# Performance work log

Hardware: AMD Instinct MI355X
Metric: run time of the kernel (lower is better)

The kernel has to match this reference:

```python
import jax, jax.numpy as jnp
import numpy as np

N = 10000       # nodes
E = 160000      # edges (avg degree 16)
IN_C = 16       # node in_channels
IN_E = 8        # edge in_edge_channels
DIMS = [32, 16, 16, 16]   # hidden_dims
ENN_H = 128     # edge_nn_hidden
EMLP_H = 16     # edge_mlp_hidden


def setup_inputs() -> dict:
    key = jax.random.key(0)
    ks = iter(jax.random.split(key, 80))
    def rn(shape, s=0.1):
        return jax.random.normal(next(ks), shape, dtype=jnp.float32) * s
    inp = {}
    inp['x'] = jax.random.normal(next(ks), (N, IN_C), dtype=jnp.float32)
    inp['edge_attr'] = jax.random.normal(next(ks), (E, IN_E), dtype=jnp.float32)
    inp['edge_index'] = jax.random.randint(next(ks), (2, E), 0, N, dtype=jnp.int32)
    in_dims = [IN_C] + DIMS[:-1]
    for i, (di, do) in enumerate(zip(in_dims, DIMS)):
        inp[f'p_w{i}'] = rn((do, di));            inp[f'p_b{i}'] = rn((do,))
        inp[f'e1_w{i}'] = rn((ENN_H, IN_E));      inp[f'e1_b{i}'] = rn((ENN_H,))
        inp[f'e2_w{i}'] = rn((do * do, ENN_H), 0.02); inp[f'e2_b{i}'] = rn((do * do,), 0.02)
        inp[f'r_w{i}'] = rn((do, do));            inp[f'c_b{i}'] = rn((do,))
    inp['m_w0'] = rn((EMLP_H, DIMS[-1])); inp['m_b0'] = rn((EMLP_H,))
    inp['m_w1'] = rn((1, EMLP_H));        inp['m_b1'] = rn((1,))
    return inp


def _forward(x, edge_attr, edge_index, params, m_w0, m_b0, m_w1, m_b1):
    row, col = edge_index[0], edge_index[1]
    n = x.shape[0]
    # in-degree for scatter-mean (clamped to 1, as PyG scatter mean)
    deg = jnp.clip(jax.ops.segment_sum(jnp.ones(row.shape[0], jnp.float32), col, num_segments=n), 1.0)
    for (pw, pb, ew1, eb1, ew2, eb2, rw, cb) in params:
        d = pw.shape[0]
        x_proj = x @ pw.T + pb                                    # [N, d]
        # edge-conditioned weight matrices: [E, d, d]
        W = (jax.nn.relu(edge_attr @ ew1.T + eb1) @ ew2.T + eb2).reshape(-1, d, d)
        msg = jnp.einsum('ei,eio->eo', x_proj[row], W)            # [E, d]
        agg = jax.ops.segment_sum(msg, col, num_segments=n) / deg[:, None]
        conv = agg + x_proj @ rw.T + cb                           # NNConv: aggr + root + bias
        x = jax.nn.relu(conv) + x_proj                            # relu + skip
    edge_repr = x[row] + x[col]                                   # [E, d_last]
    out = jax.nn.relu(edge_repr @ m_w0.T + m_b0) @ m_w1.T + m_b1  # [E, 1]
    return out[:, 0]


def reference(x, edge_attr, edge_index,
              p_w0, p_b0, e1_w0, e1_b0, e2_w0, e2_b0, r_w0, c_b0,
              p_w1, p_b1, e1_w1, e1_b1, e2_w1, e2_b1, r_w1, c_b1,
              p_w2, p_b2, e1_w2, e1_b2, e2_w2, e2_b2, r_w2, c_b2,
              p_w3, p_b3, e1_w3, e1_b3, e2_w3, e2_b3, r_w3, c_b3,
              m_w0, m_b0, m_w1, m_b1):
    params = [
        (p_w0, p_b0, e1_w0, e1_b0, e2_w0, e2_b0, r_w0, c_b0),
        (p_w1, p_b1, e1_w1, e1_b1, e2_w1, e2_b1, r_w1, c_b1),
        (p_w2, p_b2, e1_w2, e1_b2, e2_w2, e2_b2, r_w2, c_b2),
        (p_w3, p_b3, e1_w3, e1_b3, e2_w3, e2_b3, r_w3, c_b3),
    ]
    return _forward(x, edge_attr, edge_index, params, m_w0, m_b0, m_w1, m_b1)
```

## Files before the change

### kernel.cpp

```cpp
#include <hip/hip_runtime.h>

#define NN 10000
#define NE 160000
static constexpr int TPB = 256;
static constexpr int SCAN_T = 1024;

typedef unsigned int uint32;

static __device__ __forceinline__ ushort f2bf(float f) {
  uint32 u = __float_as_uint(f);
  u += 0x7fff + ((u >> 16) & 1);
  return (ushort)(u >> 16);
}
static __device__ __forceinline__ uint32 pk2bf(float a, float b) {
  return (uint32)f2bf(a) | ((uint32)f2bf(b) << 16);
}
static __device__ __forceinline__ void dot2bf(float& acc, uint32 a, uint32 b) {
  asm("v_dot2_f32_bf16 %0, %1, %2, %0" : "+v"(acc) : "v"(a), "v"(b));
}


__global__ void k_count(const int* __restrict__ ei, int* __restrict__ cnt) {
  int e = blockIdx.x * TPB + threadIdx.x;
  if (e >= NE) return;
  atomicAdd(&cnt[ei[e]], 1);
  atomicAdd(&cnt[NN + ei[NE + e]], 1);
}

__global__ void __launch_bounds__(SCAN_T)
k_scan2(const int* __restrict__ cnt_all, int* __restrict__ off_r, int* __restrict__ cur_r,
        int* __restrict__ off_c, int* __restrict__ cur_c) {
  const int* cnt = (blockIdx.x == 0) ? cnt_all : cnt_all + NN;
  int* off = (blockIdx.x == 0) ? off_r : off_c;
  int* cur = (blockIdx.x == 0) ? cur_r : cur_c;
  __shared__ int s_wave[16];
  __shared__ int s_carry;
  int tid = threadIdx.x;
  int lane = tid & 63, wid = tid >> 6;
  if (tid == 0) s_carry = 0;
  __syncthreads();
  for (int base = 0; base < NN; base += SCAN_T) {
    int i = base + tid;
    int v = (i < NN) ? cnt[i] : 0;
    int s = v;
    #pragma unroll
    for (int d = 1; d < 64; d <<= 1) {
      int t = __shfl_up(s, d, 64);
      if (lane >= d) s += t;
    }
    if (lane == 63) s_wave[wid] = s;
    __syncthreads();
    if (wid == 0 && lane < 16) {
      int ws = s_wave[lane];
      #pragma unroll
      for (int d = 1; d < 16; d <<= 1) {
        int t = __shfl_up(ws, d, 64);
        if (lane >= d) ws += t;
      }
      s_wave[lane] = ws;
    }
    __syncthreads();
    int waveoff = (wid > 0) ? s_wave[wid - 1] : 0;
    int excl = s_carry + waveoff + s - v;
    if (i < NN) { off[i] = excl; cur[i] = excl; }
    __syncthreads();
    if (tid == 0) s_carry += s_wave[15];
    __syncthreads();
  }
  if (tid == 0) off[NN] = s_carry;
}

__global__ void k_fill_row(const int* __restrict__ ei, int* __restrict__ cur_row,
                           int* __restrict__ eid_row) {
  int e = blockIdx.x * TPB + threadIdx.x;
  if (e >= NE) return;
  int r = ei[e];
  int p = atomicAdd(&cur_row[r], 1);
  eid_row[p] = e;
}

__global__ void k_fill_colpos(const int* __restrict__ ei, const int* __restrict__ eid_row,
                              int* __restrict__ cur_col, int* __restrict__ colpos) {
  int s = blockIdx.x * TPB + threadIdx.x;
  if (s >= NE) return;
  int e = eid_row[s];
  int c = ei[NE + e];
  int p = atomicAdd(&cur_col[c], 1);
  colpos[s] = p;
}


template<int DIN, int D>
__global__ void __launch_bounds__(TPB)
k_nodeprep(const float* __restrict__ x, const float* __restrict__ pw, const float* __restrict__ pb,
           const float* __restrict__ rw, const float* __restrict__ cb, const float* __restrict__ eb2,
           float* __restrict__ xp, float* __restrict__ root, float* __restrict__ Bb) {
  __shared__ float s_pw[D * DIN], s_rw[D * D], s_eb2[D * D], s_pb[D], s_cb[D];
  for (int t = threadIdx.x; t < D * DIN; t += TPB) s_pw[t] = pw[t];
  for (int t = threadIdx.x; t < D * D; t += TPB) { s_rw[t] = rw[t]; s_eb2[t] = eb2[t]; }
  for (int t = threadIdx.x; t < D; t += TPB) { s_pb[t] = pb[t]; s_cb[t] = cb[t]; }
  __syncthreads();
  int n = blockIdx.x * TPB + threadIdx.x;
  if (n >= NN) return;
  float xv[DIN];
  const float4* x4 = (const float4*)(x + (size_t)n * DIN);
  #pragma unroll
  for (int i = 0; i < DIN / 4; i++) {
    float4 v = x4[i];
    xv[4*i+0] = v.x; xv[4*i+1] = v.y; xv[4*i+2] = v.z; xv[4*i+3] = v.w;
  }
  float xpv[D];
  #pragma unroll
  for (int o = 0; o < D; o++) {
    float a = s_pb[o];
    #pragma unroll
    for (int i = 0; i < DIN; i++) a = fmaf(s_pw[o*DIN + i], xv[i], a);
    xpv[o] = a;
    xp[(size_t)n*D + o] = a;
  }
  #pragma unroll
  for (int o = 0; o < D; o++) {
    float a = s_cb[o];
    #pragma unroll
    for (int i = 0; i < D; i++) a = fmaf(s_rw[o*D + i], xpv[i], a);
    root[(size_t)n*D + o] = a;
  }
  #pragma unroll
  for (int o = 0; o < D; o++) {
    float a = 0.f;
    #pragma unroll
    for (int i = 0; i < D; i++) a = fmaf(xpv[i], s_eb2[i*D + o], a);
    Bb[(size_t)n*D + o] = a;
  }
}

template<int DP, int D>
__global__ void __launch_bounds__(TPB)
k_aggprep(const int* __restrict__ col_off,
          const float* __restrict__ msg0, const float* __restrict__ msg1,
          const float* __restrict__ root_prev, const float* __restrict__ xp_prev,
          const float* __restrict__ pw, const float* __restrict__ pb,
          const float* __restrict__ rw, const float* __restrict__ cb,
          const float* __restrict__ eb2,
          float* __restrict__ xp, float* __restrict__ root, float* __restrict__ Bb) {
  constexpr int NB = TPB / DP;
  __shared__ float s_x[NB][DP];
  __shared__ float s_xpv[NB][D];
  __shared__ float s_pw[D * DP], s_rw[D * D], s_eb2[D * D], s_pb[D], s_cb[D];
  int tid = threadIdx.x;
  for (int t = tid; t < D * DP; t += TPB) s_pw[t] = pw[t];
  for (int t = tid; t < D * D; t += TPB) { s_rw[t] = rw[t]; s_eb2[t] = eb2[t]; }
  for (int t = tid; t < D; t += TPB) { s_pb[t] = pb[t]; s_cb[t] = cb[t]; }
  int g = tid / DP, o = tid % DP;
  int n = blockIdx.x * NB + g;
  if (n < NN) {
    int p0 = col_off[n], p1 = col_off[n + 1];
    float acc = 0.f;
    for (int p = p0; p < p1; p++)
      acc += msg0[(size_t)p * DP + o] + msg1[(size_t)p * DP + o];
    float deg = (p1 > p0) ? (float)(p1 - p0) : 1.f;
    float conv = acc / deg + root_prev[(size_t)n * DP + o];
    s_x[g][o] = (conv > 0.f ? conv : 0.f) + xp_prev[(size_t)n * DP + o];
  }
  __syncthreads();
  int g2 = tid / D, o2 = tid % D;
  int n2 = blockIdx.x * NB + g2;
  if (g2 < NB && n2 < NN) {
    float a = s_pb[o2];
    #pragma unroll
    for (int i = 0; i < DP; i++) a = fmaf(s_pw[o2 * DP + i], s_x[g2][i], a);
    s_xpv[g2][o2] = a;
    xp[(size_t)n2 * D + o2] = a;
  }
  __syncthreads();
  if (g2 < NB && n2 < NN) {
    float r2 = s_cb[o2], b2 = 0.f;
    #pragma unroll
    for (int i = 0; i < D; i++) {
      r2 = fmaf(s_rw[o2 * D + i], s_xpv[g2][i], r2);
      b2 = fmaf(s_xpv[g2][i], s_eb2[i * D + o2], b2);
    }
    root[(size_t)n2 * D + o2] = r2;
    Bb[(size_t)n2 * D + o2] = b2;
  }
}

__global__ void k_trans_all(const float* __restrict__ e0, const float* __restrict__ e1,
                            const float* __restrict__ e2, const float* __restrict__ e3,
                            uint32* __restrict__ Vp) {
  int t = blockIdx.x * TPB + threadIdx.x;
  const float* ew2; uint32* dst; int D, loc;
  if (t < 65536)       { ew2 = e0; dst = Vp;         D = 32; loc = t; }
  else if (t < 81920)  { ew2 = e1; dst = Vp + 65536; D = 16; loc = t - 65536; }
  else if (t < 98304)  { ew2 = e2; dst = Vp + 81920; D = 16; loc = t - 81920; }
  else if (t < 114688) { ew2 = e3; dst = Vp + 98304; D = 16; loc = t - 98304; }
  else return;
  int COLS = D * 128;
  int i2 = loc / COLS;
  int r = loc - i2 * COLS;
  int w = r >> 1, p = r & 1;
  int k2 = w / D, o = w - k2 * D;
  int k = 2 * k2 + p;
  float lo = ew2[((size_t)((2 * i2) * D + o)) * 128 + k];
  float hi = ew2[((size_t)((2 * i2 + 1) * D + o)) * 128 + k];
  dst[loc] = pk2bf(lo, hi);
}

template<int D, int G>
__global__ void __launch_bounds__(TPB)
k_fused(const int* __restrict__ eid_row, const int* __restrict__ row_off,
        const int* __restrict__ colpos,
        const float* __restrict__ ea, const float* __restrict__ ew1,
        const float* __restrict__ eb1, const uint32* __restrict__ Vp,
        const float* __restrict__ xp, const float* __restrict__ Bb,
        float* __restrict__ msg0, float* __restrict__ msg1) {
  constexpr int OQ = D / 4;
  constexpr int EB = TPB / OQ;
  constexpr int COLS = D * 128;
  constexpr int UW = COLS / 2;
  constexpr int UH = UW / 2;
  constexpr int UP = UH + 4;
  constexpr int CT = UH / TPB;

  __shared__ __align__(16) uint32 s_w1tp[4 * 64];
  __shared__ float  s_b1[64];
  __shared__ __align__(16) uint32 s_U[G * UP];
  __shared__ __align__(16) uint32 s_hp[EB * 34];
  __shared__ __align__(16) uint32 s_eap[EB * 4];
  __shared__ int    s_cp[EB];
  __shared__ uint32 s_xp2[G][D / 2];
  __shared__ float  s_B[G * D];
  __shared__ int    s_off[G + 1];

  int tid = threadIdx.x;
  int half = blockIdx.y;
  int n0 = blockIdx.x * G;
  int GA = NN - n0; if (GA > G) GA = G;
  float* msgH = half ? msg1 : msg0;

  for (int t = tid; t < 4 * 64; t += TPB) {
    int i2 = t >> 6, kloc = t & 63;
    int k = half * 64 + kloc;
    s_w1tp[t] = pk2bf(ew1[k * 8 + 2 * i2], ew1[k * 8 + 2 * i2 + 1]);
  }
  for (int t = tid; t < 64; t += TPB) s_b1[t] = eb1[half * 64 + t];
  for (int t = tid; t < G * (D / 2); t += TPB) {
    int g = t / (D / 2), i2 = t % (D / 2);
    if (g < GA) {
      float2 v = *(const float2*)(xp + (size_t)(n0 + g) * D + 2 * i2);
      s_xp2[g][i2] = pk2bf(v.x, v.y);
    } else {
      s_xp2[g][i2] = 0;
    }
  }
  for (int t = tid; t < G * D; t += TPB) {
    int g = t / D, i = t % D;
    s_B[t] = (g < GA && half == 0) ? Bb[(size_t)(n0 + g) * D + i] : 0.f;
  }
  if (tid <= GA) s_off[tid] = row_off[n0 + tid];
  __syncthreads();

  {
    const uint2* Vp2 = (const uint2*)Vp;
    float accLo[G][CT], accHi[G][CT];
    #pragma unroll
    for (int g = 0; g < G; g++)
      #pragma unroll
      for (int j = 0; j < CT; j++) { accLo[g][j] = 0.f; accHi[g][j] = 0.f; }
    #pragma unroll 2
    for (int i2 = 0; i2 < D / 2; i2++) {
      uint2 vv[CT];
      #pragma unroll
      for (int j = 0; j < CT; j++)
        vv[j] = Vp2[(size_t)i2 * UW + half * UH + j * TPB + tid];
      #pragma unroll
      for (int g = 0; g < G; g++) {
        uint32 xg = s_xp2[g][i2];
        #pragma unroll
        for (int j = 0; j < CT; j++) {
          dot2bf(accLo[g][j], xg, vv[j].x);
          dot2bf(accHi[g][j], xg, vv[j].y);
        }
      }
    }
    #pragma unroll
    for (int g = 0; g < G; g++)
      #pragma unroll
      for (int j = 0; j < CT; j++)
        s_U[g * UP + j * TPB + tid] = pk2bf(accLo[g][j], accHi[g][j]);
  }

  int p0 = row_off[n0], p1 = row_off[n0 + GA];
  int el = tid / OQ, oq = tid % OQ;
  for (int pc = p0; pc < p1; pc += EB) {
    int cnt = p1 - pc; if (cnt > EB) cnt = EB;
    __syncthreads();
    for (int t = tid; t < cnt * 4; t += TPB) {
      int e2 = t >> 2, i2 = t & 3;
      float2 v = *(const float2*)(ea + (size_t)eid_row[pc + e2] * 8 + 2 * i2);
      s_eap[t] = pk2bf(v.x, v.y);
    }
    for (int t = tid; t < cnt; t += TPB) s_cp[t] = colpos[pc + t];
    __syncthreads();
    for (int t = tid; t < cnt * 32; t += TPB) {
      int e2 = t >> 5, k2 = t & 31;
      float a0 = s_b1[2 * k2], a1 = s_b1[2 * k2 + 1];
      #pragma unroll
      for (int i2 = 0; i2 < 4; i2++) {
        uint32 ep = s_eap[e2 * 4 + i2];
        uint2 ww = *(const uint2*)(s_w1tp + i2 * 64 + 2 * k2);
        dot2bf(a0, ep, ww.x);
        dot2bf(a1, ep, ww.y);
      }
      s_hp[e2 * 34 + k2] = pk2bf(fmaxf(a0, 0.f), fmaxf(a1, 0.f));
    }
    __syncthreads();
    if (el < cnt) {
      int s = pc + el;
      int g = 0;
      #pragma unroll
      for (int q = 1; q < G; q++) g += (q < GA && s >= s_off[q]) ? 1 : 0;
      const uint32* up = s_U + g * UP + oq * 4;
      const uint32* hp = s_hp + el * 34;
      float a0 = 0.f, a1 = 0.f, a2 = 0.f, a3 = 0.f;
      #pragma unroll 4
      for (int k4 = 0; k4 < 16; k4++) {
        uint2 hw = *(const uint2*)(hp + 2 * k4);
        uint4 u0 = *(const uint4*)(up + (2 * k4) * D);
        uint4 u1 = *(const uint4*)(up + (2 * k4 + 1) * D);
        dot2bf(a0, hw.x, u0.x); dot2bf(a1, hw.x, u0.y);
        dot2bf(a2, hw.x, u0.z); dot2bf(a3, hw.x, u0.w);
        dot2bf(a0, hw.y, u1.x); dot2bf(a1, hw.y, u1.y);
        dot2bf(a2, hw.y, u1.z); dot2bf(a3, hw.y, u1.w);
      }
      float4 b = ((const float4*)(s_B + g * D))[oq];
      float4 o4 = {a0 + b.x, a1 + b.y, a2 + b.z, a3 + b.w};
      ((float4*)(msgH + (size_t)s_cp[el] * D))[oq] = o4;
    }
  }
}

template<int D>
__global__ void __launch_bounds__(TPB)
k_agg(const int* __restrict__ col_off,
      const float* __restrict__ msg0, const float* __restrict__ msg1,
      const float* __restrict__ root, const float* __restrict__ xp,
      float* __restrict__ xout) {
  constexpr int GP = TPB / D;
  int g = threadIdx.x / D, o = threadIdx.x % D;
  int n = blockIdx.x * GP + g;
  if (n >= NN) return;
  int p0 = col_off[n], p1 = col_off[n + 1];
  float acc = 0.f;
  for (int p = p0; p < p1; p++) {
    acc += msg0[(size_t)p * D + o] + msg1[(size_t)p * D + o];
  }
  float deg = (p1 > p0) ? (float)(p1 - p0) : 1.f;
  float conv = acc / deg + root[(size_t)n * D + o];
  float rl = conv > 0.f ? conv : 0.f;
  xout[(size_t)n * D + o] = rl + xp[(size_t)n * D + o];
}

__global__ void __launch_bounds__(TPB)
k_final(const int* __restrict__ ei, const float* __restrict__ x,
        const float* __restrict__ mw0, const float* __restrict__ mb0,
        const float* __restrict__ mw1, const float* __restrict__ mb1,
        float* __restrict__ out) {
  __shared__ float s_w0[256], s_b0[16], s_w1[16], s_b1;
  for (int t = threadIdx.x; t < 256; t += TPB) s_w0[t] = mw0[t];
  if (threadIdx.x < 16) { s_b0[threadIdx.x] = mb0[threadIdx.x]; s_w1[threadIdx.x] = mw1[threadIdx.x]; }
  if (threadIdx.x == 0) s_b1 = mb1[0];
  __syncthreads();
  int e = blockIdx.x * TPB + threadIdx.x;
  if (e >= NE) return;
  int r = ei[e], c = ei[NE + e];
  const float4* xr4 = (const float4*)(x + (size_t)r * 16);
  const float4* xc4 = (const float4*)(x + (size_t)c * 16);
  float er[16];
  #pragma unroll
  for (int q = 0; q < 4; q++) {
    float4 vr = xr4[q], vc = xc4[q];
    er[4*q+0] = vr.x + vc.x; er[4*q+1] = vr.y + vc.y;
    er[4*q+2] = vr.z + vc.z; er[4*q+3] = vr.w + vc.w;
  }
  float o = s_b1;
  #pragma unroll
  for (int j = 0; j < 16; j++) {
    float t = s_b0[j];
    #pragma unroll
    for (int k = 0; k < 16; k++) t = fmaf(er[k], s_w0[j * 16 + k], t);
    t = fmaxf(t, 0.f);
    o = fmaf(t, s_w1[j], o);
  }
  out[e] = o;
}


struct LayerPtrs {
  const float *pw, *pb, *ew1, *eb1, *ew2, *eb2, *rw, *cb;
};

extern "C" void kernel_launch(void* const* d_in, const int* in_sizes, int n_in,
                              void* d_out, int out_size, void* d_ws, size_t ws_size,
                              hipStream_t stream) {
  (void)in_sizes; (void)n_in; (void)out_size; (void)ws_size;
  const float* x0 = (const float*)d_in[0];
  const float* ea = (const float*)d_in[1];
  const int* ei = (const int*)d_in[2];
  LayerPtrs L[4];
  for (int l = 0; l < 4; l++) {
    L[l].pw  = (const float*)d_in[3 + 8 * l];
    L[l].pb  = (const float*)d_in[4 + 8 * l];
    L[l].ew1 = (const float*)d_in[5 + 8 * l];
    L[l].eb1 = (const float*)d_in[6 + 8 * l];
    L[l].ew2 = (const float*)d_in[7 + 8 * l];
    L[l].eb2 = (const float*)d_in[8 + 8 * l];
    L[l].rw  = (const float*)d_in[9 + 8 * l];
    L[l].cb  = (const float*)d_in[10 + 8 * l];
  }
  const float* mw0 = (const float*)d_in[35];
  const float* mb0 = (const float*)d_in[36];
  const float* mw1 = (const float*)d_in[37];
  const float* mb1 = (const float*)d_in[38];
  float* out = (float*)d_out;

  char* w = (char*)d_ws;
  size_t off = 0;
  auto alloc = [&](size_t b) -> void* {
    void* p = w + off;
    off = (off + b + 255) & ~(size_t)255;
    return p;
  };
  int* cnt      = (int*)alloc(sizeof(int) * 2 * NN);
  int* row_off  = (int*)alloc(sizeof(int) * (NN + 1));
  int* col_off  = (int*)alloc(sizeof(int) * (NN + 1));
  int* cur_row  = (int*)alloc(sizeof(int) * NN);
  int* cur_col  = (int*)alloc(sizeof(int) * NN);
  int* eid_row  = (int*)alloc(sizeof(int) * NE);
  int* colpos   = (int*)alloc(sizeof(int) * NE);
  float* xpA   = (float*)alloc(sizeof(float) * NN * 32);
  float* xpB   = (float*)alloc(sizeof(float) * NN * 32);
  float* rootA = (float*)alloc(sizeof(float) * NN * 32);
  float* rootB = (float*)alloc(sizeof(float) * NN * 32);
  float* Bb    = (float*)alloc(sizeof(float) * NN * 32);
  float* msg0  = (float*)alloc(sizeof(float) * NE * 32);
  float* msg1  = (float*)alloc(sizeof(float) * NE * 32);
  float* xfin  = (float*)alloc(sizeof(float) * NN * 16);
  uint32* Vp   = (uint32*)alloc(sizeof(uint32) * 114688);

  hipMemsetAsync(cnt, 0, sizeof(int) * 2 * NN, stream);
  k_count<<<(NE + TPB - 1) / TPB, TPB, 0, stream>>>(ei, cnt);
  k_scan2<<<2, SCAN_T, 0, stream>>>(cnt, row_off, cur_row, col_off, cur_col);
  k_fill_row<<<(NE + TPB - 1) / TPB, TPB, 0, stream>>>(ei, cur_row, eid_row);
  k_fill_colpos<<<(NE + TPB - 1) / TPB, TPB, 0, stream>>>(ei, eid_row, cur_col, colpos);
  k_trans_all<<<(114688 + TPB - 1) / TPB, TPB, 0, stream>>>(
      L[0].ew2, L[1].ew2, L[2].ew2, L[3].ew2, Vp);

  k_nodeprep<16, 32><<<(NN + TPB - 1) / TPB, TPB, 0, stream>>>(
      x0, L[0].pw, L[0].pb, L[0].rw, L[0].cb, L[0].eb2, xpA, rootA, Bb);
  {
    dim3 gf((NN + 3) / 4, 2);
    k_fused<32, 4><<<gf, TPB, 0, stream>>>(
        eid_row, row_off, colpos, ea, L[0].ew1, L[0].eb1, Vp, xpA, Bb, msg0, msg1);
  }
  k_aggprep<32, 16><<<NN / 8, TPB, 0, stream>>>(
      col_off, msg0, msg1, rootA, xpA,
      L[1].pw, L[1].pb, L[1].rw, L[1].cb, L[1].eb2, xpB, rootB, Bb);
  {
    dim3 gf((NN + 5) / 6, 2);
    k_fused<16, 6><<<gf, TPB, 0, stream>>>(
        eid_row, row_off, colpos, ea, L[1].ew1, L[1].eb1, Vp + 65536, xpB, Bb, msg0, msg1);
  }
  k_aggprep<16, 16><<<NN / 16, TPB, 0, stream>>>(
      col_off, msg0, msg1, rootB, xpB,
      L[2].pw, L[2].pb, L[2].rw, L[2].cb, L[2].eb2, xpA, rootA, Bb);
  {
    dim3 gf((NN + 5) / 6, 2);
    k_fused<16, 6><<<gf, TPB, 0, stream>>>(
        eid_row, row_off, colpos, ea, L[2].ew1, L[2].eb1, Vp + 81920, xpA, Bb, msg0, msg1);
  }
  k_aggprep<16, 16><<<NN / 16, TPB, 0, stream>>>(
      col_off, msg0, msg1, rootA, xpA,
      L[3].pw, L[3].pb, L[3].rw, L[3].cb, L[3].eb2, xpB, rootB, Bb);
  {
    dim3 gf((NN + 5) / 6, 2);
    k_fused<16, 6><<<gf, TPB, 0, stream>>>(
        eid_row, row_off, colpos, ea, L[3].ew1, L[3].eb1, Vp + 98304, xpB, Bb, msg0, msg1);
  }
  k_agg<16><<<(NN * 16 + TPB - 1) / TPB, TPB, 0, stream>>>(
      col_off, msg0, msg1, rootB, xpB, xfin);
  k_final<<<(NE + TPB - 1) / TPB, TPB, 0, stream>>>(ei, xfin, mw0, mb0, mw1, mb1, out);
}
```

Baseline: 302.6 us.

## Store edge messages as packed bf16 and widen fused inner-loop loads

Edge messages written by the fused edge kernel are now packed as bf16 pairs instead of fp32, halving the message buffers. The aggregation kernels read and unpack them with two lanes per thread, and their launch grids are resized to match. The fused kernel's inner loop now uses 128-bit hidden-vector loads with a padded row stride, and layer 0 uses a larger node group. This cuts memory traffic on the message write/read round trip, at the cost of bf16 rounding error in the messages before they are summed.

```diff
diff --git a/kernel.cpp b/kernel.cpp
--- a/kernel.cpp
+++ b/kernel.cpp
@@ -14,6 +14,12 @@
 }
 static __device__ __forceinline__ uint32 pk2bf(float a, float b) {
   return (uint32)f2bf(a) | ((uint32)f2bf(b) << 16);
+}
+static __device__ __forceinline__ float bflo(uint32 u) {
+  return __uint_as_float(u << 16);
+}
+static __device__ __forceinline__ float bfhi(uint32 u) {
+  return __uint_as_float(u & 0xffff0000u);
 }
 static __device__ __forceinline__ void dot2bf(float& acc, uint32 a, uint32 b) {
   asm("v_dot2_f32_bf16 %0, %1, %2, %0" : "+v"(acc) : "v"(a), "v"(b));
@@ -137,13 +143,14 @@
 template<int DP, int D>
 __global__ void __launch_bounds__(TPB)
 k_aggprep(const int* __restrict__ col_off,
-          const float* __restrict__ msg0, const float* __restrict__ msg1,
+          const uint32* __restrict__ msg0p, const uint32* __restrict__ msg1p,
           const float* __restrict__ root_prev, const float* __restrict__ xp_prev,
           const float* __restrict__ pw, const float* __restrict__ pb,
           const float* __restrict__ rw, const float* __restrict__ cb,
           const float* __restrict__ eb2,
           float* __restrict__ xp, float* __restrict__ root, float* __restrict__ Bb) {
-  constexpr int NB = TPB / DP;
+  constexpr int W = DP / 2;
+  constexpr int NB = TPB / W;
   __shared__ float s_x[NB][DP];
   __shared__ float s_xpv[NB][D];
   __shared__ float s_pw[D * DP], s_rw[D * D], s_eb2[D * D], s_pb[D], s_cb[D];
@@ -151,37 +158,50 @@
   for (int t = tid; t < D * DP; t += TPB) s_pw[t] = pw[t];
   for (int t = tid; t < D * D; t += TPB) { s_rw[t] = rw[t]; s_eb2[t] = eb2[t]; }
   for (int t = tid; t < D; t += TPB) { s_pb[t] = pb[t]; s_cb[t] = cb[t]; }
-  int g = tid / DP, o = tid % DP;
+  int g = tid / W, o2 = tid % W;
   int n = blockIdx.x * NB + g;
   if (n < NN) {
     int p0 = col_off[n], p1 = col_off[n + 1];
-    float acc = 0.f;
-    for (int p = p0; p < p1; p++)
-      acc += msg0[(size_t)p * DP + o] + msg1[(size_t)p * DP + o];
+    float ax = 0.f, ay = 0.f;
+    for (int p = p0; p < p1; p++) {
+      uint32 w0 = msg0p[(size_t)p * W + o2];
+      uint32 w1 = msg1p[(size_t)p * W + o2];
+      ax += bflo(w0) + bflo(w1);
+      ay += bfhi(w0) + bfhi(w1);
+    }
     float deg = (p1 > p0) ? (float)(p1 - p0) : 1.f;
-    float conv = acc / deg + root_prev[(size_t)n * DP + o];
-    s_x[g][o] = (conv > 0.f ? conv : 0.f) + xp_prev[(size_t)n * DP + o];
+    float2 rp = *(const float2*)(root_prev + (size_t)n * DP + 2 * o2);
+    float2 xq = *(const float2*)(xp_prev + (size_t)n * DP + 2 * o2);
+    float c0 = ax / deg + rp.x, c1 = ay / deg + rp.y;
+    s_x[g][2 * o2]     = (c0 > 0.f ? c0 : 0.f) + xq.x;
+    s_x[g][2 * o2 + 1] = (c1 > 0.f ? c1 : 0.f) + xq.y;
   }
   __syncthreads();
-  int g2 = tid / D, o2 = tid % D;
-  int n2 = blockIdx.x * NB + g2;
-  if (g2 < NB && n2 < NN) {
-    float a = s_pb[o2];
-    #pragma unroll
-    for (int i = 0; i < DP; i++) a = fmaf(s_pw[o2 * DP + i], s_x[g2][i], a);
-    s_xpv[g2][o2] = a;
-    xp[(size_t)n2 * D + o2] = a;
+  for (int t = tid; t < NB * D; t += TPB) {
+    int g2 = t / D, o = t % D;
+    int n2 = blockIdx.x * NB + g2;
+    if (n2 < NN) {
+      float a = s_pb[o];
+      #pragma unroll
+      for (int i = 0; i < DP; i++) a = fmaf(s_pw[o * DP + i], s_x[g2][i], a);
+      s_xpv[g2][o] = a;
+      xp[(size_t)n2 * D + o] = a;
+    }
   }
   __syncthreads();
-  if (g2 < NB && n2 < NN) {
-    float r2 = s_cb[o2], b2 = 0.f;
-    #pragma unroll
-    for (int i = 0; i < D; i++) {
-      r2 = fmaf(s_rw[o2 * D + i], s_xpv[g2][i], r2);
-      b2 = fmaf(s_xpv[g2][i], s_eb2[i * D + o2], b2);
-    }
-    root[(size_t)n2 * D + o2] = r2;
-    Bb[(size_t)n2 * D + o2] = b2;
+  for (int t = tid; t < NB * D; t += TPB) {
+    int g2 = t / D, o = t % D;
+    int n2 = blockIdx.x * NB + g2;
+    if (n2 < NN) {
+      float r2 = s_cb[o], b2 = 0.f;
+      #pragma unroll
+      for (int i = 0; i < D; i++) {
+        r2 = fmaf(s_rw[o * D + i], s_xpv[g2][i], r2);
+        b2 = fmaf(s_xpv[g2][i], s_eb2[i * D + o], b2);
+      }
+      root[(size_t)n2 * D + o] = r2;
+      Bb[(size_t)n2 * D + o] = b2;
+    }
   }
 }
 
@@ -213,7 +233,7 @@
         const float* __restrict__ ea, const float* __restrict__ ew1,
         const float* __restrict__ eb1, const uint32* __restrict__ Vp,
         const float* __restrict__ xp, const float* __restrict__ Bb,
-        float* __restrict__ msg0, float* __restrict__ msg1) {
+        uint32* __restrict__ msg0p, uint32* __restrict__ msg1p) {
   constexpr int OQ = D / 4;
   constexpr int EB = TPB / OQ;
   constexpr int COLS = D * 128;
@@ -225,7 +245,7 @@
   __shared__ __align__(16) uint32 s_w1tp[4 * 64];
   __shared__ float  s_b1[64];
   __shared__ __align__(16) uint32 s_U[G * UP];
-  __shared__ __align__(16) uint32 s_hp[EB * 34];
+  __shared__ __align__(16) uint32 s_hp[EB * 36];
   __shared__ __align__(16) uint32 s_eap[EB * 4];
   __shared__ int    s_cp[EB];
   __shared__ uint32 s_xp2[G][D / 2];
@@ -236,7 +256,7 @@
   int half = blockIdx.y;
   int n0 = blockIdx.x * G;
   int GA = NN - n0; if (GA > G) GA = G;
-  float* msgH = half ? msg1 : msg0;
+  uint32* msgHp = half ? msg1p : msg0p;
 
   for (int t = tid; t < 4 * 64; t += TPB) {
     int i2 = t >> 6, kloc = t & 63;
@@ -312,30 +332,36 @@
         dot2bf(a0, ep, ww.x);
         dot2bf(a1, ep, ww.y);
       }
-      s_hp[e2 * 34 + k2] = pk2bf(fmaxf(a0, 0.f), fmaxf(a1, 0.f));
+      s_hp[e2 * 36 + k2] = pk2bf(fmaxf(a0, 0.f), fmaxf(a1, 0.f));
     }
     __syncthreads();
     if (el < cnt) {
-      int s = pc + el;
       int g = 0;
-      #pragma unroll
-      for (int q = 1; q < G; q++) g += (q < GA && s >= s_off[q]) ? 1 : 0;
+      {
+        int s = pc + el;
+        #pragma unroll
+        for (int q = 1; q < G; q++) g += (q < GA && s >= s_off[q]) ? 1 : 0;
+      }
       const uint32* up = s_U + g * UP + oq * 4;
-      const uint32* hp = s_hp + el * 34;
+      const uint32* hp = s_hp + el * 36;
       float a0 = 0.f, a1 = 0.f, a2 = 0.f, a3 = 0.f;
-      #pragma unroll 4
-      for (int k4 = 0; k4 < 16; k4++) {
-        uint2 hw = *(const uint2*)(hp + 2 * k4);
-        uint4 u0 = *(const uint4*)(up + (2 * k4) * D);
-        uint4 u1 = *(const uint4*)(up + (2 * k4 + 1) * D);
-        dot2bf(a0, hw.x, u0.x); dot2bf(a1, hw.x, u0.y);
-        dot2bf(a2, hw.x, u0.z); dot2bf(a3, hw.x, u0.w);
-        dot2bf(a0, hw.y, u1.x); dot2bf(a1, hw.y, u1.y);
-        dot2bf(a2, hw.y, u1.z); dot2bf(a3, hw.y, u1.w);
+      #pragma unroll
+      for (int k8 = 0; k8 < 8; k8++) {
+        uint4 hw = *(const uint4*)(hp + 4 * k8);
+        uint4 u0 = *(const uint4*)(up + (4 * k8 + 0) * D);
+        uint4 u1 = *(const uint4*)(up + (4 * k8 + 1) * D);
+        uint4 u2 = *(const uint4*)(up + (4 * k8 + 2) * D);
+        uint4 u3 = *(const uint4*)(up + (4 * k8 + 3) * D);
+        dot2bf(a0, hw.x, u0.x); dot2bf(a1, hw.x, u0.y); dot2bf(a2, hw.x, u0.z); dot2bf(a3, hw.x, u0.w);
+        dot2bf(a0, hw.y, u1.x); dot2bf(a1, hw.y, u1.y); dot2bf(a2, hw.y, u1.z); dot2bf(a3, hw.y, u1.w);
+        dot2bf(a0, hw.z, u2.x); dot2bf(a1, hw.z, u2.y); dot2bf(a2, hw.z, u2.z); dot2bf(a3, hw.z, u2.w);
+        dot2bf(a0, hw.w, u3.x); dot2bf(a1, hw.w, u3.y); dot2bf(a2, hw.w, u3.z); dot2bf(a3, hw.w, u3.w);
       }
       float4 b = ((const float4*)(s_B + g * D))[oq];
-      float4 o4 = {a0 + b.x, a1 + b.y, a2 + b.z, a3 + b.w};
-      ((float4*)(msgH + (size_t)s_cp[el] * D))[oq] = o4;
+      uint2 om;
+      om.x = pk2bf(a0 + b.x, a1 + b.y);
+      om.y = pk2bf(a2 + b.z, a3 + b.w);
+      ((uint2*)(msgHp + (size_t)s_cp[el] * (D / 2)))[oq] = om;
     }
   }
 }
@@ -343,22 +369,28 @@
 template<int D>
 __global__ void __launch_bounds__(TPB)
 k_agg(const int* __restrict__ col_off,
-      const float* __restrict__ msg0, const float* __restrict__ msg1,
+      const uint32* __restrict__ msg0p, const uint32* __restrict__ msg1p,
       const float* __restrict__ root, const float* __restrict__ xp,
       float* __restrict__ xout) {
-  constexpr int GP = TPB / D;
-  int g = threadIdx.x / D, o = threadIdx.x % D;
+  constexpr int W = D / 2;
+  constexpr int GP = TPB / W;
+  int g = threadIdx.x / W, o2 = threadIdx.x % W;
   int n = blockIdx.x * GP + g;
   if (n >= NN) return;
   int p0 = col_off[n], p1 = col_off[n + 1];
-  float acc = 0.f;
+  float ax = 0.f, ay = 0.f;
   for (int p = p0; p < p1; p++) {
-    acc += msg0[(size_t)p * D + o] + msg1[(size_t)p * D + o];
+    uint32 w0 = msg0p[(size_t)p * W + o2];
+    uint32 w1 = msg1p[(size_t)p * W + o2];
+    ax += bflo(w0) + bflo(w1);
+    ay += bfhi(w0) + bfhi(w1);
   }
   float deg = (p1 > p0) ? (float)(p1 - p0) : 1.f;
-  float conv = acc / deg + root[(size_t)n * D + o];
-  float rl = conv > 0.f ? conv : 0.f;
-  xout[(size_t)n * D + o] = rl + xp[(size_t)n * D + o];
+  float2 rp = *(const float2*)(root + (size_t)n * D + 2 * o2);
+  float2 xq = *(const float2*)(xp + (size_t)n * D + 2 * o2);
+  float c0 = ax / deg + rp.x, c1 = ay / deg + rp.y;
+  xout[(size_t)n * D + 2 * o2]     = (c0 > 0.f ? c0 : 0.f) + xq.x;
+  xout[(size_t)n * D + 2 * o2 + 1] = (c1 > 0.f ? c1 : 0.f) + xq.y;
 }
 
 __global__ void __launch_bounds__(TPB)
@@ -443,8 +475,8 @@
   float* rootA = (float*)alloc(sizeof(float) * NN * 32);
   float* rootB = (float*)alloc(sizeof(float) * NN * 32);
   float* Bb    = (float*)alloc(sizeof(float) * NN * 32);
-  float* msg0  = (float*)alloc(sizeof(float) * NE * 32);
-  float* msg1  = (float*)alloc(sizeof(float) * NE * 32);
+  uint32* msg0p = (uint32*)alloc(sizeof(uint32) * NE * 16);
+  uint32* msg1p = (uint32*)alloc(sizeof(uint32) * NE * 16);
   float* xfin  = (float*)alloc(sizeof(float) * NN * 16);
   uint32* Vp   = (uint32*)alloc(sizeof(uint32) * 114688);
 
@@ -459,35 +491,35 @@
   k_nodeprep<16, 32><<<(NN + TPB - 1) / TPB, TPB, 0, stream>>>(
       x0, L[0].pw, L[0].pb, L[0].rw, L[0].cb, L[0].eb2, xpA, rootA, Bb);
   {
-    dim3 gf((NN + 3) / 4, 2);
-    k_fused<32, 4><<<gf, TPB, 0, stream>>>(
-        eid_row, row_off, colpos, ea, L[0].ew1, L[0].eb1, Vp, xpA, Bb, msg0, msg1);
-  }
-  k_aggprep<32, 16><<<NN / 8, TPB, 0, stream>>>(
-      col_off, msg0, msg1, rootA, xpA,
+    dim3 gf((NN + 5) / 6, 2);
+    k_fused<32, 6><<<gf, TPB, 0, stream>>>(
+        eid_row, row_off, colpos, ea, L[0].ew1, L[0].eb1, Vp, xpA, Bb, msg0p, msg1p);
+  }
+  k_aggprep<32, 16><<<(NN + 15) / 16, TPB, 0, stream>>>(
+      col_off, msg0p, msg1p, rootA, xpA,
       L[1].pw, L[1].pb, L[1].rw, L[1].cb, L[1].eb2, xpB, rootB, Bb);
   {
     dim3 gf((NN + 5) / 6, 2);
     k_fused<16, 6><<<gf, TPB, 0, stream>>>(
-        eid_row, row_off, colpos, ea, L[1].ew1, L[1].eb1, Vp + 65536, xpB, Bb, msg0, msg1);
-  }
-  k_aggprep<16, 16><<<NN / 16, TPB, 0, stream>>>(
-      col_off, msg0, msg1, rootB, xpB,
+        eid_row, row_off, colpos, ea, L[1].ew1, L[1].eb1, Vp + 65536, xpB, Bb, msg0p, msg1p);
+  }
+  k_aggprep<16, 16><<<(NN + 31) / 32, TPB, 0, stream>>>(
+      col_off, msg0p, msg1p, rootB, xpB,
       L[2].pw, L[2].pb, L[2].rw, L[2].cb, L[2].eb2, xpA, rootA, Bb);
   {
     dim3 gf((NN + 5) / 6, 2);
     k_fused<16, 6><<<gf, TPB, 0, stream>>>(
-        eid_row, row_off, colpos, ea, L[2].ew1, L[2].eb1, Vp + 81920, xpA, Bb, msg0, msg1);
-  }
-  k_aggprep<16, 16><<<NN / 16, TPB, 0, stream>>>(
-      col_off, msg0, msg1, rootA, xpA,
+        eid_row, row_off, colpos, ea, L[2].ew1, L[2].eb1, Vp + 81920, xpA, Bb, msg0p, msg1p);
+  }
+  k_aggprep<16, 16><<<(NN + 31) / 32, TPB, 0, stream>>>(
+      col_off, msg0p, msg1p, rootA, xpA,
       L[3].pw, L[3].pb, L[3].rw, L[3].cb, L[3].eb2, xpB, rootB, Bb);
   {
     dim3 gf((NN + 5) / 6, 2);
     k_fused<16, 6><<<gf, TPB, 0, stream>>>(
-        eid_row, row_off, colpos, ea, L[3].ew1, L[3].eb1, Vp + 98304, xpB, Bb, msg0, msg1);
-  }
-  k_agg<16><<<(NN * 16 + TPB - 1) / TPB, TPB, 0, stream>>>(
-      col_off, msg0, msg1, rootB, xpB, xfin);
+        eid_row, row_off, colpos, ea, L[3].ew1, L[3].eb1, Vp + 98304, xpB, Bb, msg0p, msg1p);
+  }
+  k_agg<16><<<(NN + 31) / 32, TPB, 0, stream>>>(
+      col_off, msg0p, msg1p, rootB, xpB, xfin);
   k_final<<<(NE + TPB - 1) / TPB, TPB, 0, stream>>>(ei, xfin, mw0, mb0, mw1, mb1, out);
 }
```

Result: no change. 298.0 us (median of 2 runs) (-1.5%).
